# Kernel optimization log

Measured on AMD Instinct MI355X. Metric: run time of the kernel, lower is better.

The kernel has to match this reference:

```python
import jax, jax.numpy as jnp
import numpy as np

D_INNER = 5120
DT_RANK = 160
N_STATE = 16
BATCH = 256


def _softplus_thresh20(x):
    # ttnn.softplus(parameter1=1.0, parameter2=20.0): linear above threshold 20
    return jnp.where(x > 20.0, x, jnp.log1p(jnp.exp(jnp.minimum(x, 20.0))))


def setup_inputs() -> dict:
    key = jax.random.key(0)
    ks = jax.random.split(key, 9)
    x = jax.random.normal(ks[0], (1, 1, BATCH, D_INNER), dtype=jnp.float32)
    # scale weights by 1/sqrt(fan_in) so softplus input is O(1)
    W_dt_low = jax.random.normal(ks[1], (D_INNER, DT_RANK), dtype=jnp.float32) / np.sqrt(D_INNER)
    W_dt = jax.random.normal(ks[2], (DT_RANK, D_INNER), dtype=jnp.float32) / np.sqrt(DT_RANK)
    b_dt = jax.random.normal(ks[3], (D_INNER,), dtype=jnp.float32)
    W_B = jax.random.normal(ks[4], (D_INNER, N_STATE), dtype=jnp.float32) / np.sqrt(D_INNER)
    W_C = jax.random.normal(ks[5], (D_INNER, N_STATE), dtype=jnp.float32) / np.sqrt(D_INNER)
    # A = -exp(A_log): strictly negative, as in the module's preprocess_A
    A = -jnp.exp(0.5 * jax.random.normal(ks[6], (D_INNER, N_STATE), dtype=jnp.float32))
    D = jax.random.normal(ks[7], (D_INNER,), dtype=jnp.float32)
    h0 = 0.1 * jax.random.normal(ks[8], (BATCH, D_INNER, N_STATE), dtype=jnp.float32)
    return {"x": x, "W_dt_low": W_dt_low, "W_dt": W_dt, "b_dt": b_dt,
            "W_B": W_B, "W_C": W_C, "A": A, "D": D, "h0": h0}


def reference(x, W_dt_low, W_dt, b_dt, W_B, W_C, A, D, h0):
    b, d = x.shape[2], x.shape[3]
    xb = x.reshape(b, d)                                  # (B, D)
    # delta = softplus(x @ x_proj_dt @ dt_proj + bias)
    delta = _softplus_thresh20(xb @ W_dt_low @ W_dt + b_dt)   # (B, D)
    Bp = xb @ W_B                                         # (B, N)
    Cp = xb @ W_C                                         # (B, N)
    # discretize: abar = exp(delta * A), bbar = delta * B
    # layout (B, D, N) matches repeat_interleave(delta, n) / repeat(B, d)
    abar = jnp.exp(delta[:, :, None] * A[None, :, :])     # (B, D, N)
    bbar = delta[:, :, None] * Bp[:, None, :]             # (B, D, N)
    h = abar * h0 + bbar * xb[:, :, None]                 # (B, D, N)
    y = jnp.einsum('bdn,bn->bd', h, Cp)                   # reduce over state
    out = xb * D[None, :] + y                             # (B, D)
    return out.reshape(1, 1, b, d)
```

## Files before the change

### kernel.cpp

```cpp
#include <hip/hip_runtime.h>
#include <math.h>

#define D_INNER 5120
#define DT_RANK 160
#define N_STATE 16
#define BATCH   256
#define KTOT    192

#define BGRP    8
#define NBG     (BATCH / BGRP)
#define DDBLK   160
#define NDDB    (D_INNER / DDBLK)
#define SPLIT   32

#define K3_BT   2

#define OFF_T     0
#define SZ_T      (BATCH * KTOT)
#define OFF_P     (OFF_T + SZ_T)
#define SZ_P      (SPLIT * BATCH * KTOT)
#define OFF_SBC   (OFF_P + SZ_P)

__global__ __launch_bounds__(256) void k1_gemm(const float* __restrict__ x,
                                               const float* __restrict__ Wdtlow,
                                               const float* __restrict__ WB,
                                               const float* __restrict__ WC,
                                               float* __restrict__ ws) {
    __shared__ float lds[4 * BGRP * KTOT];
    const int tid  = threadIdx.x;
    const int lane = tid & 63;
    const int wv   = tid >> 6;
    const int b0   = blockIdx.x * BGRP;
    const int ddB  = blockIdx.y * DDBLK;

    float* xs = lds;
    for (int j = tid; j < (BGRP * DDBLK) / 4; j += 256) {
        int i  = j / (DDBLK / 4);
        int c4 = j % (DDBLK / 4);
        float4 v = *(const float4*)(x + (size_t)(b0 + i) * D_INNER + ddB + c4 * 4);
        *(float4*)(xs + i * DDBLK + c4 * 4) = v;
    }
    __syncthreads();

    const int dd0 = wv * 40;
    const float* p0 = Wdtlow + (size_t)(ddB + dd0) * DT_RANK + lane;
    const float* p1 = p0 + 64;
    const float* p2;
    int st2;
    if (lane < 32)      { p2 = p0 + 128;                                          st2 = DT_RANK; }
    else if (lane < 48) { p2 = WB + (size_t)(ddB + dd0) * N_STATE + (lane - 32);  st2 = N_STATE; }
    else                { p2 = WC + (size_t)(ddB + dd0) * N_STATE + (lane - 48);  st2 = N_STATE; }

    float acc0[BGRP], acc1[BGRP], acc2[BGRP];
#pragma unroll
    for (int i = 0; i < BGRP; ++i) { acc0[i] = 0.f; acc1[i] = 0.f; acc2[i] = 0.f; }

#pragma unroll 2
    for (int g = 0; g < 10; ++g) {
        float w0[4], w1[4], w2[4];
#pragma unroll
        for (int u = 0; u < 4; ++u) {
            int dd = g * 4 + u;
            w0[u] = p0[(size_t)dd * DT_RANK];
            w1[u] = p1[(size_t)dd * DT_RANK];
            w2[u] = p2[(size_t)dd * st2];
        }
#pragma unroll
        for (int i = 0; i < BGRP; ++i) {
            float4 xv = *(const float4*)(xs + i * DDBLK + dd0 + g * 4);
            acc0[i] += xv.x * w0[0] + xv.y * w0[1] + xv.z * w0[2] + xv.w * w0[3];
            acc1[i] += xv.x * w1[0] + xv.y * w1[1] + xv.z * w1[2] + xv.w * w1[3];
            acc2[i] += xv.x * w2[0] + xv.y * w2[1] + xv.z * w2[2] + xv.w * w2[3];
        }
    }
    __syncthreads();

#pragma unroll
    for (int i = 0; i < BGRP; ++i) {
        float* r = lds + wv * (BGRP * KTOT) + i * KTOT;
        r[lane]       = acc0[i];
        r[lane + 64]  = acc1[i];
        r[lane + 128] = acc2[i];
    }
    __syncthreads();

    float* P = ws + OFF_P + (size_t)blockIdx.y * (BATCH * KTOT) + (size_t)b0 * KTOT;
#pragma unroll
    for (int r = 0; r < 6; ++r) {
        int idx = tid + r * 256;
        P[idx] = lds[idx] + lds[idx + 1536] + lds[idx + 3072] + lds[idx + 4608];
    }
}

__global__ __launch_bounds__(192) void k2_reduce(float* __restrict__ ws) {
    __shared__ float ts[KTOT];
    const int b   = blockIdx.x;
    const int col = threadIdx.x;
    const float* P = ws + OFF_P + (size_t)b * KTOT + col;
    float a = 0.f;
#pragma unroll
    for (int s = 0; s < SPLIT; ++s) a += P[(size_t)s * (BATCH * KTOT)];
    ws[OFF_T + b * KTOT + col] = a;
    ts[col] = a;
    __syncthreads();
    if (col == 0) {
        float s2 = 0.f;
#pragma unroll
        for (int n = 0; n < N_STATE; ++n) s2 += ts[160 + n] * ts[176 + n];
        ws[OFF_SBC + b] = s2;
    }
}

__global__ __launch_bounds__(256, 6) void k3_fused(const float* __restrict__ Wdt,
                                                   const float* __restrict__ b_dt,
                                                   const float* __restrict__ x,
                                                   const float* __restrict__ A,
                                                   const float* __restrict__ Dv,
                                                   const float* __restrict__ h0,
                                                   const float* __restrict__ ws,
                                                   float* __restrict__ out) {
    const int tid = threadIdx.x;
    const int d   = blockIdx.x * 256 + tid;
    const int b0  = blockIdx.y * K3_BT;
    const float* T  = ws + OFF_T;
    const float* SB = ws + OFF_SBC;

    const float4* hbA = (const float4*)(h0 + ((size_t)b0 * D_INNER + d) * N_STATE);
    const float4* hbB = (const float4*)(h0 + ((size_t)(b0 + 1) * D_INNER + d) * N_STATE);
    float4 hA0 = hbA[0], hA1 = hbA[1], hA2 = hbA[2], hA3 = hbA[3];
    float4 hB0 = hbB[0], hB1 = hbB[1], hB2 = hbB[2], hB3 = hbB[3];

    float xvA = x[(size_t)b0 * D_INNER + d];
    float xvB = x[(size_t)(b0 + 1) * D_INNER + d];

    const float bdt = b_dt[d];
    const float Dd  = Dv[d];
    const float4* a4 = (const float4*)(A + (size_t)d * N_STATE);
    float4 a0 = a4[0], a1 = a4[1], a2 = a4[2], a3 = a4[3];

    const float* tA = T + (size_t)b0 * KTOT;
    const float* tB = tA + KTOT;
    float accA = 0.f, accB = 0.f;
#pragma unroll 8
    for (int k = 0; k < DT_RANK; ++k) {
        float w = Wdt[(size_t)k * D_INNER + d];
        accA += tA[k] * w;
        accB += tB[k] * w;
    }

#define SCAN_BATCH(ACC, XV, BIDX, TB, H0, H1, H2, H3)                         \
    {                                                                         \
        float v     = (ACC) + bdt;                                            \
        float delta = (v > 20.f) ? v : log1pf(__expf(v));                     \
        float sbc   = SB[BIDX];                                               \
        float y0, y1, y2, y3;                                                 \
        y0  = __expf(delta * a0.x) * H0.x * (TB)[176 + 0];                    \
        y0 += __expf(delta * a0.y) * H0.y * (TB)[176 + 1];                    \
        y0 += __expf(delta * a0.z) * H0.z * (TB)[176 + 2];                    \
        y0 += __expf(delta * a0.w) * H0.w * (TB)[176 + 3];                    \
        y1  = __expf(delta * a1.x) * H1.x * (TB)[176 + 4];                    \
        y1 += __expf(delta * a1.y) * H1.y * (TB)[176 + 5];                    \
        y1 += __expf(delta * a1.z) * H1.z * (TB)[176 + 6];                    \
        y1 += __expf(delta * a1.w) * H1.w * (TB)[176 + 7];                    \
        y2  = __expf(delta * a2.x) * H2.x * (TB)[176 + 8];                    \
        y2 += __expf(delta * a2.y) * H2.y * (TB)[176 + 9];                    \
        y2 += __expf(delta * a2.z) * H2.z * (TB)[176 + 10];                   \
        y2 += __expf(delta * a2.w) * H2.w * (TB)[176 + 11];                   \
        y3  = __expf(delta * a3.x) * H3.x * (TB)[176 + 12];                   \
        y3 += __expf(delta * a3.y) * H3.y * (TB)[176 + 13];                   \
        y3 += __expf(delta * a3.z) * H3.z * (TB)[176 + 14];                   \
        y3 += __expf(delta * a3.w) * H3.w * (TB)[176 + 15];                   \
        out[(size_t)(BIDX) * D_INNER + d] = (XV) * (Dd + delta * sbc)         \
                                          + ((y0 + y1) + (y2 + y3));          \
    }

    SCAN_BATCH(accA, xvA, b0,     tA, hA0, hA1, hA2, hA3)
    SCAN_BATCH(accB, xvB, b0 + 1, tB, hB0, hB1, hB2, hB3)
#undef SCAN_BATCH
}

extern "C" void kernel_launch(void* const* d_in, const int* in_sizes, int n_in,
                              void* d_out, int out_size, void* d_ws, size_t ws_size,
                              hipStream_t stream) {
    const float* x      = (const float*)d_in[0];
    const float* Wdtlow = (const float*)d_in[1];
    const float* Wdt    = (const float*)d_in[2];
    const float* bdt    = (const float*)d_in[3];
    const float* WB     = (const float*)d_in[4];
    const float* WC     = (const float*)d_in[5];
    const float* A      = (const float*)d_in[6];
    const float* Dv     = (const float*)d_in[7];
    const float* h0     = (const float*)d_in[8];
    float* ws  = (float*)d_ws;
    float* out = (float*)d_out;

    hipLaunchKernelGGL(k1_gemm, dim3(NBG, NDDB), dim3(256), 0, stream,
                       x, Wdtlow, WB, WC, ws);
    hipLaunchKernelGGL(k2_reduce, dim3(BATCH), dim3(192), 0, stream, ws);
    hipLaunchKernelGGL(k3_fused, dim3(D_INNER / 256, BATCH / K3_BT), dim3(256),
                       0, stream, Wdt, bdt, x, A, Dv, h0, ws, out);
}
```

Before: 183.5 us.

## Process four batches per k3 thread with double-buffered Wdt loads and staged h0 prefetch

Each k3 thread now handles four batch rows instead of two, so every Wdt element loaded from global memory feeds four dot products, halving Wdt traffic per output. The rank-160 loop is rewritten with two register buffers of eight weights that alternate, overlapping the next loads with the current FMAs. The h0 loads for the third and fourth batches are issued just before the earlier scan bodies, and sched_barriers pin that order. Occupancy is lowered to 5 waves via launch bounds to make room for the extra registers, and the grid has half as many blocks.

```diff
diff --git a/kernel.cpp b/kernel.cpp
--- a/kernel.cpp
+++ b/kernel.cpp
@@ -13,7 +13,7 @@
 #define NDDB    (D_INNER / DDBLK)
 #define SPLIT   32
 
-#define K3_BT   2
+#define K3_BT   4
 
 #define OFF_T     0
 #define SZ_T      (BATCH * KTOT)
@@ -111,7 +111,7 @@
     }
 }
 
-__global__ __launch_bounds__(256, 6) void k3_fused(const float* __restrict__ Wdt,
+__global__ __launch_bounds__(256, 5) void k3_fused(const float* __restrict__ Wdt,
                                                    const float* __restrict__ b_dt,
                                                    const float* __restrict__ x,
                                                    const float* __restrict__ A,
@@ -125,30 +125,61 @@
     const float* T  = ws + OFF_T;
     const float* SB = ws + OFF_SBC;
 
-    const float4* hbA = (const float4*)(h0 + ((size_t)b0 * D_INNER + d) * N_STATE);
-    const float4* hbB = (const float4*)(h0 + ((size_t)(b0 + 1) * D_INNER + d) * N_STATE);
-    float4 hA0 = hbA[0], hA1 = hbA[1], hA2 = hbA[2], hA3 = hbA[3];
-    float4 hB0 = hbB[0], hB1 = hbB[1], hB2 = hbB[2], hB3 = hbB[3];
-
-    float xvA = x[(size_t)b0 * D_INNER + d];
-    float xvB = x[(size_t)(b0 + 1) * D_INNER + d];
-
+    const float4* hb = (const float4*)(h0 + ((size_t)b0 * D_INNER + d) * N_STATE);
+    const size_t  hstride = (size_t)D_INNER * 4;
+
+    float4 hA0 = hb[0],           hA1 = hb[1],           hA2 = hb[2],           hA3 = hb[3];
+    float4 hB0 = hb[hstride + 0], hB1 = hb[hstride + 1], hB2 = hb[hstride + 2], hB3 = hb[hstride + 3];
+
+    float xv[K3_BT];
+#pragma unroll
+    for (int i = 0; i < K3_BT; ++i) xv[i] = x[(size_t)(b0 + i) * D_INNER + d];
+
+    const float4* a4 = (const float4*)(A + (size_t)d * N_STATE);
+    float4 a0 = a4[0], a1 = a4[1], a2 = a4[2], a3 = a4[3];
     const float bdt = b_dt[d];
     const float Dd  = Dv[d];
-    const float4* a4 = (const float4*)(A + (size_t)d * N_STATE);
-    float4 a0 = a4[0], a1 = a4[1], a2 = a4[2], a3 = a4[3];
-
+
+    __builtin_amdgcn_sched_barrier(0);
+
+    const float* wp = Wdt + d;
     const float* tA = T + (size_t)b0 * KTOT;
     const float* tB = tA + KTOT;
-    float accA = 0.f, accB = 0.f;
-#pragma unroll 8
-    for (int k = 0; k < DT_RANK; ++k) {
-        float w = Wdt[(size_t)k * D_INNER + d];
-        accA += tA[k] * w;
-        accB += tB[k] * w;
-    }
-
-#define SCAN_BATCH(ACC, XV, BIDX, TB, H0, H1, H2, H3)                         \
+    const float* tC = tB + KTOT;
+    const float* tD = tC + KTOT;
+
+    float acc0 = 0.f, acc1 = 0.f, acc2 = 0.f, acc3 = 0.f;
+    float wA[8], wB[8];
+
+#pragma unroll
+    for (int u = 0; u < 8; ++u) wA[u] = wp[(size_t)u * D_INNER];
+
+#define FMA8(TBUF, KOFF)                                                      \
+    _Pragma("unroll")                                                         \
+    for (int u = 0; u < 8; ++u) {                                             \
+        float w = TBUF[u];                                                    \
+        int   k = (KOFF) + u;                                                 \
+        acc0 += tA[k] * w;  acc1 += tB[k] * w;                                \
+        acc2 += tC[k] * w;  acc3 += tD[k] * w;                                \
+    }
+
+#pragma unroll 1
+    for (int g = 0; g < 9; ++g) {
+        const int k0 = g * 16;
+#pragma unroll
+        for (int u = 0; u < 8; ++u) wB[u] = wp[(size_t)(k0 + 8 + u) * D_INNER];
+        FMA8(wA, k0)
+#pragma unroll
+        for (int u = 0; u < 8; ++u) wA[u] = wp[(size_t)(k0 + 16 + u) * D_INNER];
+        FMA8(wB, k0 + 8)
+    }
+#pragma unroll
+    for (int u = 0; u < 8; ++u) wB[u] = wp[(size_t)(152 + u) * D_INNER];
+    FMA8(wA, 144)
+    FMA8(wB, 152)
+#undef FMA8
+
+#define SCAN_BODY(ACC, XV, BIDX, TB, H0, H1, H2, H3)                          \
     {                                                                         \
         float v     = (ACC) + bdt;                                            \
         float delta = (v > 20.f) ? v : log1pf(__expf(v));                     \
@@ -174,9 +205,19 @@
                                           + ((y0 + y1) + (y2 + y3));          \
     }
 
-    SCAN_BATCH(accA, xvA, b0,     tA, hA0, hA1, hA2, hA3)
-    SCAN_BATCH(accB, xvB, b0 + 1, tB, hB0, hB1, hB2, hB3)
-#undef SCAN_BATCH
+    const float4* hpC = hb + 2 * hstride;
+    float4 hC0 = hpC[0], hC1 = hpC[1], hC2 = hpC[2], hC3 = hpC[3];
+    __builtin_amdgcn_sched_barrier(0);
+    SCAN_BODY(acc0, xv[0], b0 + 0, tA, hA0, hA1, hA2, hA3)
+
+    const float4* hpD = hb + 3 * hstride;
+    float4 hD0 = hpD[0], hD1 = hpD[1], hD2 = hpD[2], hD3 = hpD[3];
+    __builtin_amdgcn_sched_barrier(0);
+    SCAN_BODY(acc1, xv[1], b0 + 1, tB, hB0, hB1, hB2, hB3)
+
+    SCAN_BODY(acc2, xv[2], b0 + 2, tC, hC0, hC1, hC2, hC3)
+    SCAN_BODY(acc3, xv[3], b0 + 3, tD, hD0, hD1, hD2, hD3)
+#undef SCAN_BODY
 }
 
 extern "C" void kernel_launch(void* const* d_in, const int* in_sizes, int n_in,
```

After: 189.5 us. 1.03x slower.
